# Kernel optimization log

Hardware: AMD Instinct MI355X
Metric: run time of the kernel (lower is better)

## Reference

```python
import jax, jax.numpy as jnp
import numpy as np

N_NODES = 100000
N_EDGES = 1600000
D_FEAT = 64


def setup_inputs() -> dict:
    key = jax.random.key(0)
    k1, k2 = jax.random.split(key)
    x = jax.random.normal(k1, (N_NODES, D_FEAT), dtype=jnp.float32)
    edge_index = jax.random.randint(k2, (2, N_EDGES), 0, N_NODES, dtype=jnp.int64)
    alpha = jnp.ones((), dtype=jnp.float32)
    res_scale = jnp.ones((), dtype=jnp.float32)
    return {"x": x, "alpha": alpha, "res_scale": res_scale, "edge_index": edge_index}


def reference(x, alpha, res_scale, edge_index):
    """LGConv (symmetric gcn_norm, no self-loops) -> alpha-scale -> residual.

    out_i = alpha * sum_{(j->i) in E} x_j / sqrt(deg_i * deg_j) + res_scale * x_i
    """
    n = x.shape[0]
    row, col = edge_index[0], edge_index[1]  # source, target
    # degree from target index (as in PyG gcn_norm with add_self_loops=False)
    deg = jax.ops.segment_sum(jnp.ones(row.shape[0], dtype=x.dtype), col, num_segments=n)
    deg_inv_sqrt = jnp.where(deg > 0, jax.lax.rsqrt(jnp.maximum(deg, 1.0)), 0.0)
    norm = deg_inv_sqrt[row] * deg_inv_sqrt[col]  # (E,)
    msgs = norm[:, None] * x[row]                  # (E, d) gather + scale
    out = jax.ops.segment_sum(msgs, col, num_segments=n)  # scatter-add to targets
    return alpha * out + res_scale * x
```

## Files before the change

### kernel.cpp

```cpp
#include <hip/hip_runtime.h>
#include <hip/hip_bf16.h>

#define D_FEAT 64
#define OVF_CAP 65536
#define EB 4096
#define NBMAX 1024

typedef unsigned int uint32;

__device__ inline float blo(uint32 u) { return __uint_as_float(u << 16); }
__device__ inline float bhi(uint32 u) { return __uint_as_float(u & 0xffff0000u); }
__device__ inline float dinv(int d) { return (d > 0) ? rsqrtf((float)d) : 0.0f; }

__global__ __launch_bounds__(256) void k_hist(const int* __restrict__ col,
                                              int* __restrict__ histT,
                                              const float2* __restrict__ x2,
                                              uint32* __restrict__ xb,
                                              int nhalf, int E, int B, int nb) {
    __shared__ int h[NBMAX];
    for (int i = threadIdx.x; i < nb; i += 256) h[i] = 0;
    __syncthreads();
    const int b = blockIdx.x;
    const int s = b * EB;
    const int e = (s + EB < E) ? s + EB : E;
    for (int i = s + threadIdx.x; i < e; i += 256)
        atomicAdd(&h[col[i] >> 8], 1);
    __syncthreads();
    for (int k = threadIdx.x; k < nb; k += 256)
        histT[(size_t)k * B + b] = h[k];
    const int t = b * 256 + threadIdx.x;
    const int stride = B * 256;
    for (int j = t; j < nhalf; j += stride) {
        float2 v = x2[j];
        __hip_bfloat16 bx = __float2bfloat16(v.x);
        __hip_bfloat16 by = __float2bfloat16(v.y);
        uint32 ux = *reinterpret_cast<unsigned short*>(&bx);
        uint32 uy = *reinterpret_cast<unsigned short*>(&by);
        xb[j] = ux | (uy << 16);
    }
}

__global__ __launch_bounds__(512) void k_colscan(int* __restrict__ histT,
                                                 int* __restrict__ total, int B) {
    __shared__ int sh[512];
    const int k = blockIdx.x;
    int v = (threadIdx.x < B) ? histT[(size_t)k * B + threadIdx.x] : 0;
    sh[threadIdx.x] = v;
    __syncthreads();
    for (int off = 1; off < 512; off <<= 1) {
        int t = (threadIdx.x >= off) ? sh[threadIdx.x - off] : 0;
        __syncthreads();
        sh[threadIdx.x] += t;
        __syncthreads();
    }
    int incl = sh[threadIdx.x];
    if (threadIdx.x < B) histT[(size_t)k * B + threadIdx.x] = incl - v;
    if (threadIdx.x == 511) total[k] = incl;
}

__global__ __launch_bounds__(1024) void k_tinyscan(const int* __restrict__ total,
                                                   int* __restrict__ bstart, int nb) {
    __shared__ int sh[1024];
    int v = (threadIdx.x < nb) ? total[threadIdx.x] : 0;
    sh[threadIdx.x] = v;
    __syncthreads();
    for (int off = 1; off < 1024; off <<= 1) {
        int t = (threadIdx.x >= off) ? sh[threadIdx.x - off] : 0;
        __syncthreads();
        sh[threadIdx.x] += t;
        __syncthreads();
    }
    if (threadIdx.x < nb) bstart[threadIdx.x] = sh[threadIdx.x] - v;
    if (threadIdx.x == nb - 1) bstart[nb] = sh[threadIdx.x];
}

__global__ __launch_bounds__(256) void k_scat3(const int* __restrict__ row,
                                               const int* __restrict__ col,
                                               const int* __restrict__ histT,
                                               const int* __restrict__ bstart,
                                               uint32* __restrict__ binned,
                                               int E, int B, int nb) {
    __shared__ int cur[NBMAX];
    const int b = blockIdx.x;
    for (int k = threadIdx.x; k < nb; k += 256)
        cur[k] = bstart[k] + histT[(size_t)k * B + b];
    __syncthreads();
    const int s = b * EB;
    const int e = (s + EB < E) ? s + EB : E;
    for (int i = s + threadIdx.x; i < e; i += 256) {
        int c = col[i];
        uint32 r = (uint32)row[i];
        int pos = atomicAdd(&cur[c >> 8], 1);
        binned[pos] = (r << 8) | (uint32)(c & 255);
    }
}

__global__ __launch_bounds__(1024) void k_build(const int* __restrict__ bstart,
                                                const uint32* __restrict__ binned,
                                                int* __restrict__ slots,
                                                int* __restrict__ deg,
                                                int2* __restrict__ ovf,
                                                int* __restrict__ ovf_cnt,
                                                int n, int C) {
    __shared__ int cnt[256];
    const int k = blockIdx.x;
    if (threadIdx.x < 256) cnt[threadIdx.x] = 0;
    __syncthreads();
    const int s = bstart[k], e = bstart[k + 1];
    const int base = k << 8;
    for (int i = s + threadIdx.x; i < e; i += 1024) {
        uint32 pk = binned[i];
        int cl = (int)(pk & 255);
        int r  = (int)(pk >> 8);
        int rk = atomicAdd(&cnt[cl], 1);
        int c  = base + cl;
        if (rk < C) {
            slots[(size_t)c * C + rk] = r;
        } else {
            int o = atomicAdd(ovf_cnt, 1);
            if (o < OVF_CAP) ovf[o] = make_int2(r, c);
        }
    }
    __syncthreads();
    int i = base + threadIdx.x;
    if (threadIdx.x < 256 && i < n) deg[i] = cnt[threadIdx.x];
}

__global__ void k_gather4(const uint32* __restrict__ xb,
                          const float4* __restrict__ x4,
                          const int* __restrict__ deg,
                          const int* __restrict__ slots,
                          const float* __restrict__ alpha_p,
                          const float* __restrict__ rs_p,
                          float4* __restrict__ out4, int n, int C) {
    int wid = (blockIdx.x * blockDim.x + threadIdx.x) >> 6;
    if (wid >= n) return;
    const int lane = threadIdx.x & 63;
    const int q = lane >> 4;
    const int l = lane & 15;
    int d = deg[wid];
    int e = (d < C) ? d : C;
    const int* sl = slots + (size_t)wid * C;
    float ax = 0.f, ay = 0.f, az = 0.f, aw = 0.f;
    int k = 0;
    for (; k + 16 <= e; k += 16) {
        int s0 = sl[k + q];
        int s1 = sl[k + 4 + q];
        int s2 = sl[k + 8 + q];
        int s3 = sl[k + 12 + q];
        int d0 = deg[s0], d1 = deg[s1], d2 = deg[s2], d3 = deg[s3];
        uint2 p0 = ((const uint2*)(xb + (size_t)s0 * 32))[l];
        uint2 p1 = ((const uint2*)(xb + (size_t)s1 * 32))[l];
        uint2 p2 = ((const uint2*)(xb + (size_t)s2 * 32))[l];
        uint2 p3 = ((const uint2*)(xb + (size_t)s3 * 32))[l];
        float w0 = dinv(d0), w1 = dinv(d1), w2 = dinv(d2), w3 = dinv(d3);
        ax = fmaf(w0, blo(p0.x), ax); ay = fmaf(w0, bhi(p0.x), ay);
        az = fmaf(w0, blo(p0.y), az); aw = fmaf(w0, bhi(p0.y), aw);
        ax = fmaf(w1, blo(p1.x), ax); ay = fmaf(w1, bhi(p1.x), ay);
        az = fmaf(w1, blo(p1.y), az); aw = fmaf(w1, bhi(p1.y), aw);
        ax = fmaf(w2, blo(p2.x), ax); ay = fmaf(w2, bhi(p2.x), ay);
        az = fmaf(w2, blo(p2.y), az); aw = fmaf(w2, bhi(p2.y), aw);
        ax = fmaf(w3, blo(p3.x), ax); ay = fmaf(w3, bhi(p3.x), ay);
        az = fmaf(w3, blo(p3.y), az); aw = fmaf(w3, bhi(p3.y), aw);
    }
    for (; k < e; k += 4) {
        int kk = k + q;
        if (kk < e) {
            int s0 = sl[kk];
            float w0 = dinv(deg[s0]);
            uint2 p0 = ((const uint2*)(xb + (size_t)s0 * 32))[l];
            ax = fmaf(w0, blo(p0.x), ax); ay = fmaf(w0, bhi(p0.x), ay);
            az = fmaf(w0, blo(p0.y), az); aw = fmaf(w0, bhi(p0.y), aw);
        }
    }
    ax += __shfl_down(ax, 32, 64); ay += __shfl_down(ay, 32, 64);
    az += __shfl_down(az, 32, 64); aw += __shfl_down(aw, 32, 64);
    ax += __shfl_down(ax, 16, 64); ay += __shfl_down(ay, 16, 64);
    az += __shfl_down(az, 16, 64); aw += __shfl_down(aw, 16, 64);
    if (q == 0) {
        float adw = (*alpha_p) * dinv(d);
        float rs  = *rs_p;
        float4 xr = x4[(size_t)wid * 16 + l];
        float4 o;
        o.x = fmaf(adw, ax, rs * xr.x);
        o.y = fmaf(adw, ay, rs * xr.y);
        o.z = fmaf(adw, az, rs * xr.z);
        o.w = fmaf(adw, aw, rs * xr.w);
        out4[(size_t)wid * 16 + l] = o;
    }
}

__global__ void k_ovf(const int2* __restrict__ ovf, const int* __restrict__ cnt_p,
                      const float* __restrict__ x, const int* __restrict__ deg,
                      const float* __restrict__ alpha_p, float* __restrict__ out) {
    int cnt = *cnt_p;
    if (cnt > OVF_CAP) cnt = OVF_CAP;
    if (cnt <= 0) return;
    float a = *alpha_p;
    long long total = (long long)cnt * 64;
    long long stride = (long long)gridDim.x * blockDim.x;
    for (long long idx = blockIdx.x * (long long)blockDim.x + threadIdx.x;
         idx < total; idx += stride) {
        int e = (int)(idx >> 6);
        int f = (int)(idx & 63);
        int2 rc = ovf[e];
        float w = a * dinv(deg[rc.x]) * dinv(deg[rc.y]);
        atomicAdd(&out[(size_t)rc.y * D_FEAT + f], w * x[(size_t)rc.x * D_FEAT + f]);
    }
}

__global__ void k_prep(const float2* __restrict__ x2, uint32* __restrict__ xb,
                       const int* __restrict__ row, const int* __restrict__ col,
                       int* __restrict__ deg, int* __restrict__ slots,
                       int2* __restrict__ ovf, int* __restrict__ ovf_cnt,
                       int nhalf, int E, int C) {
    int t = blockIdx.x * blockDim.x + threadIdx.x;
    if (t < E) {
        int c = col[t];
        int r = row[t];
        int rk = atomicAdd(&deg[c], 1);
        if (rk < C) {
            slots[(size_t)c * C + rk] = r;
        } else {
            int o = atomicAdd(ovf_cnt, 1);
            if (o < OVF_CAP) ovf[o] = make_int2(r, c);
        }
    }
    const int stride = gridDim.x * blockDim.x;
    for (int j = t; j < nhalf; j += stride) {
        float2 v = x2[j];
        __hip_bfloat16 bx = __float2bfloat16(v.x);
        __hip_bfloat16 by = __float2bfloat16(v.y);
        uint32 ux = *reinterpret_cast<unsigned short*>(&bx);
        uint32 uy = *reinterpret_cast<unsigned short*>(&by);
        xb[j] = ux | (uy << 16);
    }
}

static inline char* align_up(char* p, size_t a) {
    return (char*)(((uintptr_t)p + (a - 1)) & ~(uintptr_t)(a - 1));
}

extern "C" void kernel_launch(void* const* d_in, const int* in_sizes, int n_in,
                              void* d_out, int out_size, void* d_ws, size_t ws_size,
                              hipStream_t stream) {
    const float* x         = (const float*)d_in[0];
    const float* alpha     = (const float*)d_in[1];
    const float* res_scale = (const float*)d_in[2];
    const int*   ei        = (const int*)d_in[3];

    const int n = in_sizes[0] / D_FEAT;
    const int E = in_sizes[3] / 2;
    const int* row = ei;
    const int* col = ei + E;

    float* out = (float*)d_out;
    const int nhalf = n * (D_FEAT / 2);
    const int nb = (n + 255) >> 8;
    const int B  = (E + EB - 1) / EB;

    {
        char* p = (char*)d_ws;
        int*    deg     = (int*)p;            p += (size_t)n * 4;
        int*    ovf_cnt = (int*)p;            p += 4;
        int2*   ovf     = (int2*)p;           p += (size_t)OVF_CAP * 8;
        int*    histT   = (int*)p;            p += (size_t)nb * B * 4;
        int*    total   = (int*)p;            p += (size_t)nb * 4;
        int*    bstart  = (int*)p;            p += (size_t)(nb + 1) * 4;
        p = align_up(p, 16);
        uint32* xb      = (uint32*)p;         p += (size_t)n * 128;
        uint32* binned  = (uint32*)p;         p += (size_t)E * 4;
        int*    slots   = (int*)p;
        const size_t fixed = (size_t)(p - (char*)d_ws);

        int C = 0;
        if (ws_size > fixed) {
            size_t c_avail = (ws_size - fixed) / ((size_t)n * 4);
            C = (c_avail > 32) ? 32 : (int)c_avail;
        }
        const bool ok = (C >= 16) && (nb <= NBMAX) && (B <= 512) &&
                        (n <= (NBMAX << 8));
        if (ok) {
            hipMemsetAsync(ovf_cnt, 0, 4, stream);
            k_hist    <<<B, 256, 0, stream>>>(col, histT, (const float2*)x, xb,
                                              nhalf, E, B, nb);
            k_colscan <<<nb, 512, 0, stream>>>(histT, total, B);
            k_tinyscan<<<1, 1024, 0, stream>>>(total, bstart, nb);
            k_scat3   <<<B, 256, 0, stream>>>(row, col, histT, bstart, binned,
                                              E, B, nb);
            k_build   <<<nb, 1024, 0, stream>>>(bstart, binned, slots, deg,
                                                ovf, ovf_cnt, n, C);
            const long long tt = (long long)n * D_FEAT;
            const int blocks = (int)((tt + 255) / 256);
            k_gather4<<<blocks, 256, 0, stream>>>(xb, (const float4*)x, deg, slots,
                                                  alpha, res_scale, (float4*)out,
                                                  n, C);
            k_ovf<<<64, 256, 0, stream>>>(ovf, ovf_cnt, x, deg, alpha, out);
            return;
        }
    }

    {
        char* p = (char*)d_ws;
        int*    deg     = (int*)p;            p += (size_t)n * 4;
        int*    ovf_cnt = (int*)p;            p += 4;
        int2*   ovf     = (int2*)p;           p += (size_t)OVF_CAP * 8;
        p = align_up(p, 16);
        uint32* xb      = (uint32*)p;         p += (size_t)n * 128;
        int*    slots   = (int*)p;
        const size_t fixed = (size_t)(p - (char*)d_ws);
        int C = 0;
        if (ws_size > fixed) {
            size_t c_avail = (ws_size - fixed) / ((size_t)n * 4);
            C = (c_avail > 32) ? 32 : (int)c_avail;
        }
        if (C < 1) return;
        hipMemsetAsync(deg, 0, (size_t)n * 4 + 4, stream);
        k_prep<<<(E + 255) / 256, 256, 0, stream>>>(
            (const float2*)x, xb, row, col, deg, slots, ovf, ovf_cnt,
            nhalf, E, C);
        const long long tt = (long long)n * D_FEAT;
        const int blocks = (int)((tt + 255) / 256);
        k_gather4<<<blocks, 256, 0, stream>>>(xb, (const float4*)x, deg, slots,
                                              alpha, res_scale, (float4*)out, n, C);
        k_ovf<<<64, 256, 0, stream>>>(ovf, ovf_cnt, x, deg, alpha, out);
    }
}
```

Measured before the change: 186.7 us.

## Split bf16 feature table into four column slices for cache-local gather

The bf16 copy of x is now stored as four feature slices of 16 columns each, laid out slice-major. The gather kernel runs one block per (4-node chunk, slice), so each slice's 3.2MB working set can stay resident in cache while neighbour rows are fetched. Each wave now processes 16 neighbours per iteration with 4 lanes per neighbour, and the reduction gains two shuffle levels. The cost is that slot indices and degrees are re-read once per slice, and each row fetch shrinks to 32 bytes.

```diff
diff --git a/kernel.cpp b/kernel.cpp
--- a/kernel.cpp
+++ b/kernel.cpp
@@ -5,6 +5,7 @@
 #define OVF_CAP 65536
 #define EB 4096
 #define NBMAX 1024
+#define NSLICE 4
 
 typedef unsigned int uint32;
 
@@ -16,7 +17,8 @@
                                               int* __restrict__ histT,
                                               const float2* __restrict__ x2,
                                               uint32* __restrict__ xb,
-                                              int nhalf, int E, int B, int nb) {
+                                              int nhalf, int E, int B, int nb,
+                                              int n) {
     __shared__ int h[NBMAX];
     for (int i = threadIdx.x; i < nb; i += 256) h[i] = 0;
     __syncthreads();
@@ -36,7 +38,12 @@
         __hip_bfloat16 by = __float2bfloat16(v.y);
         uint32 ux = *reinterpret_cast<unsigned short*>(&bx);
         uint32 uy = *reinterpret_cast<unsigned short*>(&by);
-        xb[j] = ux | (uy << 16);
+        uint32 u = ux | (uy << 16);
+        int node = j >> 5;
+        int p = j & 31;
+        int slice = p >> 3;
+        int fp = p & 7;
+        xb[((size_t)slice * n + node) * 8 + fp] = u;
     }
 }
 
@@ -126,49 +133,43 @@
     if (threadIdx.x < 256 && i < n) deg[i] = cnt[threadIdx.x];
 }
 
-__global__ void k_gather4(const uint32* __restrict__ xb,
-                          const float4* __restrict__ x4,
-                          const int* __restrict__ deg,
-                          const int* __restrict__ slots,
-                          const float* __restrict__ alpha_p,
-                          const float* __restrict__ rs_p,
-                          float4* __restrict__ out4, int n, int C) {
-    int wid = (blockIdx.x * blockDim.x + threadIdx.x) >> 6;
-    if (wid >= n) return;
+__global__ __launch_bounds__(256) void k_gather_s(const uint2* __restrict__ xbs,
+                                                  const float4* __restrict__ x4,
+                                                  const int* __restrict__ deg,
+                                                  const int* __restrict__ slots,
+                                                  const float* __restrict__ alpha_p,
+                                                  const float* __restrict__ rs_p,
+                                                  float4* __restrict__ out4,
+                                                  int n, int C) {
+    const int slice = blockIdx.x & (NSLICE - 1);
+    const int chunk = blockIdx.x >> 2;
+    const int wv = threadIdx.x >> 6;
+    const int node = chunk * 4 + wv;
+    if (node >= n) return;
     const int lane = threadIdx.x & 63;
-    const int q = lane >> 4;
-    const int l = lane & 15;
-    int d = deg[wid];
+    const int q = lane >> 2;
+    const int l = lane & 3;
+    int d = deg[node];
     int e = (d < C) ? d : C;
-    const int* sl = slots + (size_t)wid * C;
+    const int* sl = slots + (size_t)node * C;
+    float4 xr = make_float4(0.f, 0.f, 0.f, 0.f);
+    if (q == 0) xr = x4[(size_t)node * 16 + slice * 4 + l];
     float ax = 0.f, ay = 0.f, az = 0.f, aw = 0.f;
+    const size_t sb = (size_t)slice * n;
     int k = 0;
     for (; k + 16 <= e; k += 16) {
         int s0 = sl[k + q];
-        int s1 = sl[k + 4 + q];
-        int s2 = sl[k + 8 + q];
-        int s3 = sl[k + 12 + q];
-        int d0 = deg[s0], d1 = deg[s1], d2 = deg[s2], d3 = deg[s3];
-        uint2 p0 = ((const uint2*)(xb + (size_t)s0 * 32))[l];
-        uint2 p1 = ((const uint2*)(xb + (size_t)s1 * 32))[l];
-        uint2 p2 = ((const uint2*)(xb + (size_t)s2 * 32))[l];
-        uint2 p3 = ((const uint2*)(xb + (size_t)s3 * 32))[l];
-        float w0 = dinv(d0), w1 = dinv(d1), w2 = dinv(d2), w3 = dinv(d3);
+        float w0 = dinv(deg[s0]);
+        uint2 p0 = xbs[(sb + s0) * 4 + l];
         ax = fmaf(w0, blo(p0.x), ax); ay = fmaf(w0, bhi(p0.x), ay);
         az = fmaf(w0, blo(p0.y), az); aw = fmaf(w0, bhi(p0.y), aw);
-        ax = fmaf(w1, blo(p1.x), ax); ay = fmaf(w1, bhi(p1.x), ay);
-        az = fmaf(w1, blo(p1.y), az); aw = fmaf(w1, bhi(p1.y), aw);
-        ax = fmaf(w2, blo(p2.x), ax); ay = fmaf(w2, bhi(p2.x), ay);
-        az = fmaf(w2, blo(p2.y), az); aw = fmaf(w2, bhi(p2.y), aw);
-        ax = fmaf(w3, blo(p3.x), ax); ay = fmaf(w3, bhi(p3.x), ay);
-        az = fmaf(w3, blo(p3.y), az); aw = fmaf(w3, bhi(p3.y), aw);
-    }
-    for (; k < e; k += 4) {
+    }
+    if (k < e) {
         int kk = k + q;
         if (kk < e) {
             int s0 = sl[kk];
             float w0 = dinv(deg[s0]);
-            uint2 p0 = ((const uint2*)(xb + (size_t)s0 * 32))[l];
+            uint2 p0 = xbs[(sb + s0) * 4 + l];
             ax = fmaf(w0, blo(p0.x), ax); ay = fmaf(w0, bhi(p0.x), ay);
             az = fmaf(w0, blo(p0.y), az); aw = fmaf(w0, bhi(p0.y), aw);
         }
@@ -177,16 +178,19 @@
     az += __shfl_down(az, 32, 64); aw += __shfl_down(aw, 32, 64);
     ax += __shfl_down(ax, 16, 64); ay += __shfl_down(ay, 16, 64);
     az += __shfl_down(az, 16, 64); aw += __shfl_down(aw, 16, 64);
+    ax += __shfl_down(ax,  8, 64); ay += __shfl_down(ay,  8, 64);
+    az += __shfl_down(az,  8, 64); aw += __shfl_down(aw,  8, 64);
+    ax += __shfl_down(ax,  4, 64); ay += __shfl_down(ay,  4, 64);
+    az += __shfl_down(az,  4, 64); aw += __shfl_down(aw,  4, 64);
     if (q == 0) {
         float adw = (*alpha_p) * dinv(d);
         float rs  = *rs_p;
-        float4 xr = x4[(size_t)wid * 16 + l];
         float4 o;
         o.x = fmaf(adw, ax, rs * xr.x);
         o.y = fmaf(adw, ay, rs * xr.y);
         o.z = fmaf(adw, az, rs * xr.z);
         o.w = fmaf(adw, aw, rs * xr.w);
-        out4[(size_t)wid * 16 + l] = o;
+        out4[(size_t)node * 16 + slice * 4 + l] = o;
     }
 }
 
@@ -213,7 +217,7 @@
                        const int* __restrict__ row, const int* __restrict__ col,
                        int* __restrict__ deg, int* __restrict__ slots,
                        int2* __restrict__ ovf, int* __restrict__ ovf_cnt,
-                       int nhalf, int E, int C) {
+                       int nhalf, int E, int C, int n) {
     int t = blockIdx.x * blockDim.x + threadIdx.x;
     if (t < E) {
         int c = col[t];
@@ -233,7 +237,12 @@
         __hip_bfloat16 by = __float2bfloat16(v.y);
         uint32 ux = *reinterpret_cast<unsigned short*>(&bx);
         uint32 uy = *reinterpret_cast<unsigned short*>(&by);
-        xb[j] = ux | (uy << 16);
+        uint32 u = ux | (uy << 16);
+        int node = j >> 5;
+        int p = j & 31;
+        int slice = p >> 3;
+        int fp = p & 7;
+        xb[((size_t)slice * n + node) * 8 + fp] = u;
     }
 }
 
@@ -283,18 +292,17 @@
         if (ok) {
             hipMemsetAsync(ovf_cnt, 0, 4, stream);
             k_hist    <<<B, 256, 0, stream>>>(col, histT, (const float2*)x, xb,
-                                              nhalf, E, B, nb);
+                                              nhalf, E, B, nb, n);
             k_colscan <<<nb, 512, 0, stream>>>(histT, total, B);
             k_tinyscan<<<1, 1024, 0, stream>>>(total, bstart, nb);
             k_scat3   <<<B, 256, 0, stream>>>(row, col, histT, bstart, binned,
                                               E, B, nb);
             k_build   <<<nb, 1024, 0, stream>>>(bstart, binned, slots, deg,
                                                 ovf, ovf_cnt, n, C);
-            const long long tt = (long long)n * D_FEAT;
-            const int blocks = (int)((tt + 255) / 256);
-            k_gather4<<<blocks, 256, 0, stream>>>(xb, (const float4*)x, deg, slots,
-                                                  alpha, res_scale, (float4*)out,
-                                                  n, C);
+            const int gblocks = ((n + 3) >> 2) * NSLICE;
+            k_gather_s<<<gblocks, 256, 0, stream>>>((const uint2*)xb, (const float4*)x,
+                                                    deg, slots, alpha, res_scale,
+                                                    (float4*)out, n, C);
             k_ovf<<<64, 256, 0, stream>>>(ovf, ovf_cnt, x, deg, alpha, out);
             return;
         }
@@ -318,11 +326,11 @@
         hipMemsetAsync(deg, 0, (size_t)n * 4 + 4, stream);
         k_prep<<<(E + 255) / 256, 256, 0, stream>>>(
             (const float2*)x, xb, row, col, deg, slots, ovf, ovf_cnt,
-            nhalf, E, C);
-        const long long tt = (long long)n * D_FEAT;
-        const int blocks = (int)((tt + 255) / 256);
-        k_gather4<<<blocks, 256, 0, stream>>>(xb, (const float4*)x, deg, slots,
-                                              alpha, res_scale, (float4*)out, n, C);
+            nhalf, E, C, n);
+        const int gblocks = ((n + 3) >> 2) * NSLICE;
+        k_gather_s<<<gblocks, 256, 0, stream>>>((const uint2*)xb, (const float4*)x,
+                                                deg, slots, alpha, res_scale,
+                                                (float4*)out, n, C);
         k_ovf<<<64, 256, 0, stream>>>(ovf, ovf_cnt, x, deg, alpha, out);
     }
 }
```

Measured after the change: 247.8 us. +32.8%, slower.
